# Optimization experiments

Measured on AMD Instinct MI355X. Metric: run time of the kernel, lower is better.

Reference implementation:

```python
import jax, jax.numpy as jnp
import numpy as np

E = 800_000      # number of edges
DIN = 128        # in_channels
DMID = 256       # mid_channels
DOUT = 128       # output_channels
V = 50_000       # number of vertices (segments)


def setup_inputs() -> dict:
    key = jax.random.key(0)
    k1, k2, k3, k4, k5 = jax.random.split(key, 5)
    x = jax.random.normal(k1, (E, DIN), dtype=jnp.float32)
    vertex_id = jax.random.randint(k2, (E,), 0, V)
    W1 = jax.random.normal(k3, (DIN, DMID), dtype=jnp.float32) * (1.0 / np.sqrt(DIN))
    b1 = jax.random.normal(k4, (DMID,), dtype=jnp.float32) * 0.01
    W2 = jax.random.normal(k5, (DIN + DMID, DOUT), dtype=jnp.float32) * (1.0 / np.sqrt(DIN + DMID))
    return {"x": x, "vertex_id": vertex_id, "W1": W1, "b1": b1, "W2": W2, "num_vertices": V}


def reference(x, vertex_id, W1, b1, W2, num_vertices):
    # first_process: Linear(DIN -> DMID)                        (E, DMID)
    z = x @ W1 + b1
    # aggregator: scatter_max over vertex segments              (V, DMID)
    z_max = jax.ops.segment_max(z, vertex_id, num_segments=num_vertices)
    # formatter: index_select gather back to edges              (E, DMID)
    z_vertex = jnp.take(z_max, vertex_id, axis=0)
    # merger: concat along feature dim                          (E, DIN+DMID)
    z_merged = jnp.concatenate([x, z_vertex], axis=-1)
    # second_process: Linear(DIN+DMID -> DOUT, bias=False)      (E, DOUT)
    return z_merged @ W2
```

## Files before the change

kernel.cpp:

```cpp
#include <hip/hip_runtime.h>

#define DIN   128
#define DMID  256
#define DOUT  128
#define VNUM  50000

typedef __attribute__((ext_vector_type(8))) __bf16 bf16x8;
typedef __attribute__((ext_vector_type(4))) float  f32x4;

static __device__ __forceinline__ unsigned flipf(float f) {
  unsigned u = __float_as_uint(f);
  return u ^ ((unsigned)((int)u >> 31) | 0x80000000u);
}
static __device__ __forceinline__ unsigned unflip_bits(unsigned m) {
  unsigned mask = ((int)m < 0) ? 0x80000000u : 0xFFFFFFFFu;
  return m ^ mask;
}
static __device__ __forceinline__ unsigned short flip16(unsigned short b) {
  return b ^ (unsigned short)(((short)b >> 15) | 0x8000);
}
static __device__ __forceinline__ unsigned flip32_from16(unsigned short m) {
  return ((unsigned)m << 16) | ((m & 0x8000u) ? 0u : 0xFFFFu);
}
static __device__ __forceinline__ unsigned short f2b_bits(unsigned b) {
  return (unsigned short)((b + 0x7FFFu + ((b >> 16) & 1u)) >> 16);
}
static __device__ __forceinline__ unsigned short f2b(float f) {
  return f2b_bits(__float_as_uint(f));
}

__global__ void k_hist(const int* __restrict__ vid, int* __restrict__ counts, int E) {
  int i = blockIdx.x * blockDim.x + threadIdx.x;
  if (i < E) atomicAdd(counts + vid[i], 1);
}

__global__ __launch_bounds__(1024) void k_scan(int* __restrict__ cursor, int V) {
  __shared__ int wsum[16];
  const int tid = threadIdx.x, lane = tid & 63, wv = tid >> 6;
  int carry = 0;
  for (int base = 0; base < V; base += 1024) {
    const int idx = base + tid;
    const int c = (idx < V) ? cursor[idx] : 0;
    int s = c;
#pragma unroll
    for (int d = 1; d < 64; d <<= 1) {
      int t = __shfl_up(s, d, 64);
      if (lane >= d) s += t;
    }
    if (lane == 63) wsum[wv] = s;
    __syncthreads();
    if (wv == 0 && lane < 16) {
      int ws = wsum[lane];
#pragma unroll
      for (int d = 1; d < 16; d <<= 1) {
        int t = __shfl_up(ws, d, 16);
        if (lane >= d) ws += t;
      }
      wsum[lane] = ws;
    }
    __syncthreads();
    const int woff = (wv == 0) ? 0 : wsum[wv - 1];
    if (idx < V) cursor[idx] = carry + woff + (s - c);
    carry += wsum[15];
    __syncthreads();
  }
}

__global__ void k_scatter(const int* __restrict__ vid, int* __restrict__ cursor,
                          int* __restrict__ sorted, int E) {
  int i = blockIdx.x * blockDim.x + threadIdx.x;
  if (i < E) {
    int v = vid[i];
    int p = atomicAdd(cursor + v, 1);
    sorted[p] = i;
  }
}

__global__ __launch_bounds__(256, 3) void k_gemm1_max(
    const float* __restrict__ x, const int* __restrict__ vid,
    const int* __restrict__ sorted, const float* __restrict__ W1,
    const float* __restrict__ b1, unsigned* __restrict__ zu, int ntiles) {
  __shared__ unsigned short lx[64 * 136];
  __shared__ unsigned short zt[64 * 266];
  __shared__ int lvid[64];
  __shared__ int leid[64];

  const int tid  = threadIdx.x;
  const int lane = tid & 63;
  const int w    = tid >> 6;
  const int l15  = lane & 15;
  const int l4   = lane >> 4;

  bf16x8 bfrag[4][4];
  float  bias[4];
#pragma unroll
  for (int ni = 0; ni < 4; ++ni) {
    const int col = w * 64 + ni * 16 + l15;
    bias[ni] = b1[col];
#pragma unroll
    for (int kk = 0; kk < 4; ++kk) {
      union { bf16x8 v; unsigned short u[8]; } tmp;
#pragma unroll
      for (int j = 0; j < 8; ++j)
        tmp.u[j] = f2b(W1[(kk * 32 + l4 * 8 + j) * DMID + col]);
      bfrag[kk][ni] = tmp.v;
    }
  }

  for (int t = blockIdx.x; t < ntiles; t += gridDim.x) {
    if (tid < 64) {
      const int e = sorted[t * 64 + tid];
      leid[tid] = e;
      lvid[tid] = vid[e];
    }
    __syncthreads();

    {
      const int row = tid >> 2, q = tid & 3;
      const float4* src =
          reinterpret_cast<const float4*>(x + (size_t)leid[row] * DIN + q * 32);
      unsigned short* dst = &lx[row * 136 + q * 32];
#pragma unroll
      for (int i = 0; i < 8; ++i) {
        float4 v = src[i];
        ushort4 o = { f2b(v.x), f2b(v.y), f2b(v.z), f2b(v.w) };
        *reinterpret_cast<ushort4*>(dst + i * 4) = o;
      }
    }
    __syncthreads();

    f32x4 acc[4][4];
#pragma unroll
    for (int mi = 0; mi < 4; ++mi)
#pragma unroll
      for (int ni = 0; ni < 4; ++ni)
        acc[mi][ni] = (f32x4){bias[ni], bias[ni], bias[ni], bias[ni]};
#pragma unroll
    for (int kk = 0; kk < 4; ++kk) {
      bf16x8 a[4];
#pragma unroll
      for (int mi = 0; mi < 4; ++mi)
        a[mi] = *reinterpret_cast<const bf16x8*>(
            &lx[(mi * 16 + l15) * 136 + kk * 32 + l4 * 8]);
#pragma unroll
      for (int mi = 0; mi < 4; ++mi)
#pragma unroll
        for (int ni = 0; ni < 4; ++ni)
          acc[mi][ni] = __builtin_amdgcn_mfma_f32_16x16x32_bf16(
              a[mi], bfrag[kk][ni], acc[mi][ni], 0, 0, 0);
    }

#pragma unroll
    for (int mi = 0; mi < 4; ++mi)
#pragma unroll
      for (int ni = 0; ni < 4; ++ni)
#pragma unroll
        for (int r = 0; r < 4; ++r) {
          const int row = mi * 16 + l4 * 4 + r;
          const int col = w * 64 + ni * 16 + l15;
          zt[row * 266 + col] = flip16(f2b(acc[mi][ni][r]));
        }
    __syncthreads();

    {
      const int col = tid;
      unsigned short cur = zt[col];
      int curv = lvid[0];
#pragma unroll 4
      for (int rr = 1; rr < 64; ++rr) {
        const unsigned short val = zt[rr * 266 + col];
        const int vv = lvid[rr];
        if (vv != curv) {
          atomicMax(zu + (size_t)curv * DMID + col, flip32_from16(cur));
          curv = vv;
          cur = val;
        } else {
          cur = (val > cur) ? val : cur;
        }
      }
      atomicMax(zu + (size_t)curv * DMID + col, flip32_from16(cur));
    }
    __syncthreads();
  }
}

__global__ __launch_bounds__(256) void k_ymm(
    const unsigned* __restrict__ zu, const float* __restrict__ W2,
    float* __restrict__ Y, int ntiles) {
  extern __shared__ unsigned short sm[];
  unsigned short* w2bt = sm;
  unsigned short* za   = sm + 128 * 264;

  const int tid  = threadIdx.x;
  const int lane = tid & 63;
  const int w    = tid >> 6;
  const int wr   = w >> 1, wc = w & 1;
  const int l15  = lane & 15, l4 = lane >> 4;

  {
    const int n = tid & 127, kh = tid >> 7;
    for (int k = kh * 128; k < kh * 128 + 128; ++k)
      w2bt[n * 264 + k] = f2b(W2[(size_t)(DIN + k) * DOUT + n]);
  }
  __syncthreads();

  for (int t = blockIdx.x; t < ntiles; t += gridDim.x) {
    {
      const int row = tid >> 2, q = tid & 3;
      const int v = t * 64 + row;
      unsigned short* dz = &za[row * 264 + q * 64];
      if (v < VNUM) {
        const uint4* sz = reinterpret_cast<const uint4*>(zu + (size_t)v * DMID + q * 64);
#pragma unroll
        for (int i = 0; i < 16; ++i) {
          uint4 m = sz[i];
          ushort4 o = { (unsigned short)(unflip_bits(m.x) >> 16),
                        (unsigned short)(unflip_bits(m.y) >> 16),
                        (unsigned short)(unflip_bits(m.z) >> 16),
                        (unsigned short)(unflip_bits(m.w) >> 16) };
          *reinterpret_cast<ushort4*>(dz + i * 4) = o;
        }
      } else {
        ushort4 zo = {0, 0, 0, 0};
#pragma unroll
        for (int i = 0; i < 16; ++i) *reinterpret_cast<ushort4*>(dz + i * 4) = zo;
      }
    }
    __syncthreads();

    f32x4 acc[2][4];
#pragma unroll
    for (int mi = 0; mi < 2; ++mi)
#pragma unroll
      for (int ni = 0; ni < 4; ++ni) acc[mi][ni] = (f32x4){0.f, 0.f, 0.f, 0.f};

#pragma unroll
    for (int kk = 0; kk < 8; ++kk) {
      bf16x8 a[2], b[4];
#pragma unroll
      for (int mi = 0; mi < 2; ++mi)
        a[mi] = *reinterpret_cast<const bf16x8*>(
            &za[(wr * 32 + mi * 16 + l15) * 264 + kk * 32 + l4 * 8]);
#pragma unroll
      for (int ni = 0; ni < 4; ++ni)
        b[ni] = *reinterpret_cast<const bf16x8*>(
            &w2bt[(wc * 64 + ni * 16 + l15) * 264 + kk * 32 + l4 * 8]);
#pragma unroll
      for (int mi = 0; mi < 2; ++mi)
#pragma unroll
        for (int ni = 0; ni < 4; ++ni)
          acc[mi][ni] = __builtin_amdgcn_mfma_f32_16x16x32_bf16(
              a[mi], b[ni], acc[mi][ni], 0, 0, 0);
    }

#pragma unroll
    for (int mi = 0; mi < 2; ++mi)
#pragma unroll
      for (int r = 0; r < 4; ++r) {
        const int v = t * 64 + wr * 32 + mi * 16 + l4 * 4 + r;
        if (v < VNUM) {
          float* o = Y + (size_t)v * DOUT + wc * 64 + l15;
#pragma unroll
          for (int ni = 0; ni < 4; ++ni) o[ni * 16] = acc[mi][ni][r];
        }
      }
    __syncthreads();
  }
}

__global__ __launch_bounds__(256, 3) void k_gemm2(
    const float* __restrict__ x, const int* __restrict__ vid,
    const float* __restrict__ W2, const float* __restrict__ Y,
    float* __restrict__ out, int ntiles) {
  __shared__ unsigned short w2at[128 * 136];
  __shared__ unsigned short lx[64 * 136];
  __shared__ int lvid[64];

  const int tid  = threadIdx.x;
  const int lane = tid & 63;
  const int w    = tid >> 6;
  const int wr   = w >> 1, wc = w & 1;
  const int l15  = lane & 15, l4 = lane >> 4;

  {
    const int n = tid & 127, kh = tid >> 7;
    for (int k = kh * 64; k < kh * 64 + 64; ++k)
      w2at[n * 136 + k] = f2b(W2[(size_t)k * DOUT + n]);
  }
  __syncthreads();

  for (int t = blockIdx.x; t < ntiles; t += gridDim.x) {
    {
      const int row = tid >> 2, q = tid & 3;
      const float4* sx =
          reinterpret_cast<const float4*>(x + (size_t)(t * 64 + row) * DIN + q * 32);
      unsigned short* dx = &lx[row * 136 + q * 32];
#pragma unroll
      for (int i = 0; i < 8; ++i) {
        float4 v = sx[i];
        ushort4 o = { f2b(v.x), f2b(v.y), f2b(v.z), f2b(v.w) };
        *reinterpret_cast<ushort4*>(dx + i * 4) = o;
      }
      if (tid < 64) lvid[tid] = vid[t * 64 + tid];
    }
    __syncthreads();

    f32x4 acc[2][4];
#pragma unroll
    for (int mi = 0; mi < 2; ++mi)
#pragma unroll
      for (int ni = 0; ni < 4; ++ni) acc[mi][ni] = (f32x4){0.f, 0.f, 0.f, 0.f};

#pragma unroll
    for (int kk = 0; kk < 4; ++kk) {
      bf16x8 a[2], b[4];
#pragma unroll
      for (int mi = 0; mi < 2; ++mi)
        a[mi] = *reinterpret_cast<const bf16x8*>(
            &lx[(wr * 32 + mi * 16 + l15) * 136 + kk * 32 + l4 * 8]);
#pragma unroll
      for (int ni = 0; ni < 4; ++ni)
        b[ni] = *reinterpret_cast<const bf16x8*>(
            &w2at[(wc * 64 + ni * 16 + l15) * 136 + kk * 32 + l4 * 8]);
#pragma unroll
      for (int mi = 0; mi < 2; ++mi)
#pragma unroll
        for (int ni = 0; ni < 4; ++ni)
          acc[mi][ni] = __builtin_amdgcn_mfma_f32_16x16x32_bf16(
              a[mi], b[ni], acc[mi][ni], 0, 0, 0);
    }

#pragma unroll
    for (int mi = 0; mi < 2; ++mi)
#pragma unroll
      for (int r = 0; r < 4; ++r) {
        const int row = wr * 32 + mi * 16 + l4 * 4 + r;
        const float* Yr = Y + (size_t)lvid[row] * DOUT + wc * 64 + l15;
        float* o = out + (size_t)(t * 64 + row) * DOUT + wc * 64 + l15;
#pragma unroll
        for (int ni = 0; ni < 4; ++ni) o[ni * 16] = acc[mi][ni][r] + Yr[ni * 16];
      }
    __syncthreads();
  }
}

extern "C" void kernel_launch(void* const* d_in, const int* in_sizes, int n_in,
                              void* d_out, int out_size, void* d_ws, size_t ws_size,
                              hipStream_t stream) {
  const float* x   = (const float*)d_in[0];
  const int*   vid = (const int*)d_in[1];
  const float* W1  = (const float*)d_in[2];
  const float* b1  = (const float*)d_in[3];
  const float* W2  = (const float*)d_in[4];
  float* out = (float*)d_out;

  const int E = in_sizes[1];
  const int ntiles = E / 64;
  const int ntY = (VNUM + 63) / 64;

  char* ws = (char*)d_ws;
  unsigned* zu   = (unsigned*)ws;
  int* cnt       = (int*)(ws + (size_t)VNUM * DMID * 4);
  int* sorted    = (int*)(ws + (size_t)VNUM * DMID * 4 + VNUM * 4);
  float* Y       = (float*)(ws + (size_t)VNUM * DMID * 4 + VNUM * 4 + (size_t)E * 4);

  hipMemsetAsync(zu, 0, (size_t)VNUM * DMID * 4 + VNUM * 4, stream);

  k_hist<<<(E + 255) / 256, 256, 0, stream>>>(vid, cnt, E);
  k_scan<<<1, 1024, 0, stream>>>(cnt, VNUM);
  k_scatter<<<(E + 255) / 256, 256, 0, stream>>>(vid, cnt, sorted, E);

  k_gemm1_max<<<768, 256, 0, stream>>>(x, vid, sorted, W1, b1, zu, ntiles);

  const int smY = (128 * 264 + 64 * 264) * sizeof(unsigned short);
  hipFuncSetAttribute((const void*)k_ymm,
                      hipFuncAttributeMaxDynamicSharedMemorySize, smY);
  k_ymm<<<256, 256, smY, stream>>>(zu, W2, Y, ntY);

  k_gemm2<<<768, 256, 0, stream>>>(x, vid, W2, Y, out, ntiles);
}
```

Baseline: 619.0 us.

## Prefetch next tile in registers and reduce segment max in registers

In both edge GEMM kernels, the next tile's x rows and vertex ids are now loaded into registers while the current tile's MFMAs run, so global-load latency overlaps compute. In gemm1 the segment max uses register fmax plus lane shuffles instead of staging through a shared z tile. Vertex runs that lie fully inside a tile are written with plain stores, and only runs at tile edges use atomicMax. The Y gather in gemm2 is hoisted ahead of the MFMAs, launch-bounds occupancy hints are dropped, and k_ymm gets enough blocks to cover all vertex tiles. The trade-off is higher register pressure, which may lower occupancy.

```diff
diff --git a/kernel.cpp b/kernel.cpp
--- a/kernel.cpp
+++ b/kernel.cpp
@@ -8,10 +8,6 @@
 typedef __attribute__((ext_vector_type(8))) __bf16 bf16x8;
 typedef __attribute__((ext_vector_type(4))) float  f32x4;
 
-static __device__ __forceinline__ unsigned flipf(float f) {
-  unsigned u = __float_as_uint(f);
-  return u ^ ((unsigned)((int)u >> 31) | 0x80000000u);
-}
 static __device__ __forceinline__ unsigned unflip_bits(unsigned m) {
   unsigned mask = ((int)m < 0) ? 0x80000000u : 0xFFFFFFFFu;
   return m ^ mask;
@@ -27,6 +23,9 @@
 }
 static __device__ __forceinline__ unsigned short f2b(float f) {
   return f2b_bits(__float_as_uint(f));
+}
+static __device__ __forceinline__ unsigned enc_max(float m) {
+  return flip32_from16(flip16(f2b(m)));
 }
 
 __global__ void k_hist(const int* __restrict__ vid, int* __restrict__ counts, int E) {
@@ -76,20 +75,21 @@
   }
 }
 
-__global__ __launch_bounds__(256, 3) void k_gemm1_max(
+__global__ __launch_bounds__(256) void k_gemm1_max(
     const float* __restrict__ x, const int* __restrict__ vid,
     const int* __restrict__ sorted, const float* __restrict__ W1,
     const float* __restrict__ b1, unsigned* __restrict__ zu, int ntiles) {
   __shared__ unsigned short lx[64 * 136];
-  __shared__ unsigned short zt[64 * 266];
   __shared__ int lvid[64];
-  __shared__ int leid[64];
 
   const int tid  = threadIdx.x;
   const int lane = tid & 63;
   const int w    = tid >> 6;
   const int l15  = lane & 15;
   const int l4   = lane >> 4;
+  const int row4 = tid >> 2;
+  const int q    = tid & 3;
+  const int G    = gridDim.x;
 
   bf16x8 bfrag[4][4];
   float  bias[4];
@@ -107,27 +107,36 @@
     }
   }
 
-  for (int t = blockIdx.x; t < ntiles; t += gridDim.x) {
-    if (tid < 64) {
-      const int e = sorted[t * 64 + tid];
-      leid[tid] = e;
-      lvid[tid] = vid[e];
-    }
-    __syncthreads();
-
-    {
-      const int row = tid >> 2, q = tid & 3;
-      const float4* src =
-          reinterpret_cast<const float4*>(x + (size_t)leid[row] * DIN + q * 32);
-      unsigned short* dst = &lx[row * 136 + q * 32];
-#pragma unroll
-      for (int i = 0; i < 8; ++i) {
-        float4 v = src[i];
-        ushort4 o = { f2b(v.x), f2b(v.y), f2b(v.z), f2b(v.w) };
-        *reinterpret_cast<ushort4*>(dst + i * 4) = o;
-      }
-    }
-    __syncthreads();
+  const int t0 = blockIdx.x;
+  if (t0 >= ntiles) return;
+
+  {
+    const int eid = sorted[t0 * 64 + row4];
+    const float4* src = reinterpret_cast<const float4*>(x + (size_t)eid * DIN + q * 32);
+    unsigned short* dst = &lx[row4 * 136 + q * 32];
+#pragma unroll
+    for (int i = 0; i < 8; ++i) {
+      float4 v = src[i];
+      ushort4 o = { f2b(v.x), f2b(v.y), f2b(v.z), f2b(v.w) };
+      *reinterpret_cast<ushort4*>(dst + i * 4) = o;
+    }
+    if (tid < 64) lvid[tid] = vid[sorted[t0 * 64 + tid]];
+  }
+  int tn0 = t0 + G; if (tn0 >= ntiles) tn0 = t0;
+  int eidN   = sorted[tn0 * 64 + row4];
+  int eidN64 = (tid < 64) ? sorted[tn0 * 64 + tid] : 0;
+  __syncthreads();
+
+  for (int t = t0; t < ntiles; t += G) {
+    int tn = t + G; if (tn >= ntiles) tn = t;
+
+    float4 xn[8];
+    {
+      const float4* src = reinterpret_cast<const float4*>(x + (size_t)eidN * DIN + q * 32);
+#pragma unroll
+      for (int i = 0; i < 8; ++i) xn[i] = src[i];
+    }
+    int vN = (tid < 64) ? vid[eidN64] : 0;
 
     f32x4 acc[4][4];
 #pragma unroll
@@ -150,36 +159,58 @@
               a[mi], bfrag[kk][ni], acc[mi][ni], 0, 0, 0);
     }
 
-#pragma unroll
-    for (int mi = 0; mi < 4; ++mi)
-#pragma unroll
-      for (int ni = 0; ni < 4; ++ni)
-#pragma unroll
-        for (int r = 0; r < 4; ++r) {
-          const int row = mi * 16 + l4 * 4 + r;
-          const int col = w * 64 + ni * 16 + l15;
-          zt[row * 266 + col] = flip16(f2b(acc[mi][ni][r]));
+    {
+      int rs = 0;
+      while (rs < 64) {
+        const int v = lvid[rs];
+        int re = rs + 1;
+        while (re < 64 && lvid[re] == v) ++re;
+
+        float mx[4];
+#pragma unroll
+        for (int ni = 0; ni < 4; ++ni) mx[ni] = -3.4e38f;
+#pragma unroll
+        for (int mi = 0; mi < 4; ++mi)
+#pragma unroll
+          for (int r = 0; r < 4; ++r) {
+            const int row = mi * 16 + l4 * 4 + r;
+            const bool in = (row >= rs) && (row < re);
+#pragma unroll
+            for (int ni = 0; ni < 4; ++ni)
+              mx[ni] = in ? fmaxf(mx[ni], acc[mi][ni][r]) : mx[ni];
+          }
+#pragma unroll
+        for (int ni = 0; ni < 4; ++ni) {
+          mx[ni] = fmaxf(mx[ni], __shfl_xor(mx[ni], 16));
+          mx[ni] = fmaxf(mx[ni], __shfl_xor(mx[ni], 32));
         }
-    __syncthreads();
-
-    {
-      const int col = tid;
-      unsigned short cur = zt[col];
-      int curv = lvid[0];
-#pragma unroll 4
-      for (int rr = 1; rr < 64; ++rr) {
-        const unsigned short val = zt[rr * 266 + col];
-        const int vv = lvid[rr];
-        if (vv != curv) {
-          atomicMax(zu + (size_t)curv * DMID + col, flip32_from16(cur));
-          curv = vv;
-          cur = val;
-        } else {
-          cur = (val > cur) ? val : cur;
+        const bool boundary = (rs == 0) || (re == 64);
+        if (l4 == 0) {
+          unsigned* base = zu + (size_t)v * DMID + w * 64 + l15;
+#pragma unroll
+          for (int ni = 0; ni < 4; ++ni) {
+            const unsigned e = enc_max(mx[ni]);
+            if (boundary) atomicMax(base + ni * 16, e);
+            else          base[ni * 16] = e;
+          }
         }
-      }
-      atomicMax(zu + (size_t)curv * DMID + col, flip32_from16(cur));
-    }
+        rs = re;
+      }
+    }
+    __syncthreads();
+
+    {
+      unsigned short* dst = &lx[row4 * 136 + q * 32];
+#pragma unroll
+      for (int i = 0; i < 8; ++i) {
+        ushort4 o = { f2b(xn[i].x), f2b(xn[i].y), f2b(xn[i].z), f2b(xn[i].w) };
+        *reinterpret_cast<ushort4*>(dst + i * 4) = o;
+      }
+      if (tid < 64) lvid[tid] = vN;
+    }
+    int t2 = tn + G; if (t2 >= ntiles) t2 = tn;
+    eidN   = sorted[t2 * 64 + row4];
+    eidN64 = (tid < 64) ? sorted[t2 * 64 + tid] : 0;
     __syncthreads();
   }
 }
@@ -268,7 +299,7 @@
   }
 }
 
-__global__ __launch_bounds__(256, 3) void k_gemm2(
+__global__ __launch_bounds__(256) void k_gemm2(
     const float* __restrict__ x, const int* __restrict__ vid,
     const float* __restrict__ W2, const float* __restrict__ Y,
     float* __restrict__ out, int ntiles) {
@@ -281,36 +312,65 @@
   const int w    = tid >> 6;
   const int wr   = w >> 1, wc = w & 1;
   const int l15  = lane & 15, l4 = lane >> 4;
+  const int row4 = tid >> 2, q = tid & 3;
+  const int G    = gridDim.x;
 
   {
     const int n = tid & 127, kh = tid >> 7;
     for (int k = kh * 64; k < kh * 64 + 64; ++k)
       w2at[n * 136 + k] = f2b(W2[(size_t)k * DOUT + n]);
   }
+
+  const int t0 = blockIdx.x;
+  if (t0 >= ntiles) return;
+
+  float4 xr[8];
+  {
+    const float4* src =
+        reinterpret_cast<const float4*>(x + (size_t)(t0 * 64 + row4) * DIN + q * 32);
+#pragma unroll
+    for (int i = 0; i < 8; ++i) xr[i] = src[i];
+  }
+  int vOwn = (tid < 64) ? vid[t0 * 64 + tid] : 0;
   __syncthreads();
 
-  for (int t = blockIdx.x; t < ntiles; t += gridDim.x) {
-    {
-      const int row = tid >> 2, q = tid & 3;
-      const float4* sx =
-          reinterpret_cast<const float4*>(x + (size_t)(t * 64 + row) * DIN + q * 32);
-      unsigned short* dx = &lx[row * 136 + q * 32];
+  for (int t = t0; t < ntiles; t += G) {
+    {
+      unsigned short* dst = &lx[row4 * 136 + q * 32];
 #pragma unroll
       for (int i = 0; i < 8; ++i) {
-        float4 v = sx[i];
-        ushort4 o = { f2b(v.x), f2b(v.y), f2b(v.z), f2b(v.w) };
-        *reinterpret_cast<ushort4*>(dx + i * 4) = o;
-      }
-      if (tid < 64) lvid[tid] = vid[t * 64 + tid];
-    }
-    __syncthreads();
+        ushort4 o = { f2b(xr[i].x), f2b(xr[i].y), f2b(xr[i].z), f2b(xr[i].w) };
+        *reinterpret_cast<ushort4*>(dst + i * 4) = o;
+      }
+      if (tid < 64) lvid[tid] = vOwn;
+    }
+    __syncthreads();
+
+    int tn = t + G; if (tn >= ntiles) tn = t;
+    {
+      const float4* src =
+          reinterpret_cast<const float4*>(x + (size_t)(tn * 64 + row4) * DIN + q * 32);
+#pragma unroll
+      for (int i = 0; i < 8; ++i) xr[i] = src[i];
+    }
+    vOwn = (tid < 64) ? vid[tn * 64 + tid] : 0;
+
+    float yv[2][4][4];
+#pragma unroll
+    for (int mi = 0; mi < 2; ++mi)
+#pragma unroll
+      for (int r = 0; r < 4; ++r) {
+        const int row = wr * 32 + mi * 16 + l4 * 4 + r;
+        const float* Yr = Y + (size_t)lvid[row] * DOUT + wc * 64 + l15;
+#pragma unroll
+        for (int ni = 0; ni < 4; ++ni) yv[mi][r][ni] = Yr[ni * 16];
+      }
 
     f32x4 acc[2][4];
 #pragma unroll
     for (int mi = 0; mi < 2; ++mi)
 #pragma unroll
       for (int ni = 0; ni < 4; ++ni) acc[mi][ni] = (f32x4){0.f, 0.f, 0.f, 0.f};
-
 #pragma unroll
     for (int kk = 0; kk < 4; ++kk) {
       bf16x8 a[2], b[4];
@@ -335,10 +395,9 @@
 #pragma unroll
       for (int r = 0; r < 4; ++r) {
         const int row = wr * 32 + mi * 16 + l4 * 4 + r;
-        const float* Yr = Y + (size_t)lvid[row] * DOUT + wc * 64 + l15;
         float* o = out + (size_t)(t * 64 + row) * DOUT + wc * 64 + l15;
 #pragma unroll
-        for (int ni = 0; ni < 4; ++ni) o[ni * 16] = acc[mi][ni][r] + Yr[ni * 16];
+        for (int ni = 0; ni < 4; ++ni) o[ni * 16] = acc[mi][ni][r] + yv[mi][r][ni];
       }
     __syncthreads();
   }
@@ -359,10 +418,10 @@
   const int ntY = (VNUM + 63) / 64;
 
   char* ws = (char*)d_ws;
-  unsigned* zu   = (unsigned*)ws;
-  int* cnt       = (int*)(ws + (size_t)VNUM * DMID * 4);
-  int* sorted    = (int*)(ws + (size_t)VNUM * DMID * 4 + VNUM * 4);
-  float* Y       = (float*)(ws + (size_t)VNUM * DMID * 4 + VNUM * 4 + (size_t)E * 4);
+  unsigned* zu = (unsigned*)ws;
+  int* cnt     = (int*)(ws + (size_t)VNUM * DMID * 4);
+  int* sorted  = (int*)(ws + (size_t)VNUM * DMID * 4 + VNUM * 4);
+  float* Y     = (float*)(ws + (size_t)VNUM * DMID * 4 + VNUM * 4 + (size_t)E * 4);
 
   hipMemsetAsync(zu, 0, (size_t)VNUM * DMID * 4 + VNUM * 4, stream);
 
@@ -375,7 +434,7 @@
   const int smY = (128 * 264 + 64 * 264) * sizeof(unsigned short);
   hipFuncSetAttribute((const void*)k_ymm,
                       hipFuncAttributeMaxDynamicSharedMemorySize, smY);
-  k_ymm<<<256, 256, smY, stream>>>(zu, W2, Y, ntY);
+  k_ymm<<<782, 256, smY, stream>>>(zu, W2, Y, ntY);
 
   k_gemm2<<<768, 256, 0, stream>>>(x, vid, W2, Y, out, ntiles);
 }
```

Result: slower. 939.0 us (+51.7%).

## Reduce segment max in registers via ballot runs and widen gemm1 blocks

Applied to the files above, without the earlier changes.

The first GEMM kernel now uses 512-thread blocks with 8 waves, each owning 32 output columns, and drops the LDS staging tile for the segment max. Segment boundaries are found with a wave ballot over the sorted vertex ids. Each run is reduced in registers with cross-lane shuffles, and interior runs are written with a plain store, while only runs touching the tile edges use atomicMax. The aim is to cut LDS traffic, a barrier and most of the atomics, at the cost of a serial loop over runs that is replicated in every wave. The grid sizes for gemm1 and k_ymm are also raised.

```diff
diff --git a/kernel.cpp b/kernel.cpp
--- a/kernel.cpp
+++ b/kernel.cpp
@@ -8,10 +8,6 @@
 typedef __attribute__((ext_vector_type(8))) __bf16 bf16x8;
 typedef __attribute__((ext_vector_type(4))) float  f32x4;
 
-static __device__ __forceinline__ unsigned flipf(float f) {
-  unsigned u = __float_as_uint(f);
-  return u ^ ((unsigned)((int)u >> 31) | 0x80000000u);
-}
 static __device__ __forceinline__ unsigned unflip_bits(unsigned m) {
   unsigned mask = ((int)m < 0) ? 0x80000000u : 0xFFFFFFFFu;
   return m ^ mask;
@@ -27,6 +23,9 @@
 }
 static __device__ __forceinline__ unsigned short f2b(float f) {
   return f2b_bits(__float_as_uint(f));
+}
+static __device__ __forceinline__ unsigned enc_max(float m) {
+  return flip32_from16(flip16(f2b(m)));
 }
 
 __global__ void k_hist(const int* __restrict__ vid, int* __restrict__ counts, int E) {
@@ -76,26 +75,26 @@
   }
 }
 
-__global__ __launch_bounds__(256, 3) void k_gemm1_max(
+__global__ __launch_bounds__(512, 4) void k_gemm1_max(
     const float* __restrict__ x, const int* __restrict__ vid,
     const int* __restrict__ sorted, const float* __restrict__ W1,
     const float* __restrict__ b1, unsigned* __restrict__ zu, int ntiles) {
   __shared__ unsigned short lx[64 * 136];
-  __shared__ unsigned short zt[64 * 266];
   __shared__ int lvid[64];
-  __shared__ int leid[64];
 
   const int tid  = threadIdx.x;
   const int lane = tid & 63;
   const int w    = tid >> 6;
   const int l15  = lane & 15;
   const int l4   = lane >> 4;
-
-  bf16x8 bfrag[4][4];
-  float  bias[4];
-#pragma unroll
-  for (int ni = 0; ni < 4; ++ni) {
-    const int col = w * 64 + ni * 16 + l15;
+  const int row8 = tid >> 3;
+  const int s8   = tid & 7;
+
+  bf16x8 bfrag[4][2];
+  float  bias[2];
+#pragma unroll
+  for (int ni = 0; ni < 2; ++ni) {
+    const int col = w * 32 + ni * 16 + l15;
     bias[ni] = b1[col];
 #pragma unroll
     for (int kk = 0; kk < 4; ++kk) {
@@ -108,20 +107,14 @@
   }
 
   for (int t = blockIdx.x; t < ntiles; t += gridDim.x) {
-    if (tid < 64) {
-      const int e = sorted[t * 64 + tid];
-      leid[tid] = e;
-      lvid[tid] = vid[e];
-    }
-    __syncthreads();
-
+    if (tid < 64) lvid[tid] = vid[sorted[t * 64 + tid]];
     {
-      const int row = tid >> 2, q = tid & 3;
+      const int eid = sorted[t * 64 + row8];
       const float4* src =
-          reinterpret_cast<const float4*>(x + (size_t)leid[row] * DIN + q * 32);
-      unsigned short* dst = &lx[row * 136 + q * 32];
-#pragma unroll
-      for (int i = 0; i < 8; ++i) {
+          reinterpret_cast<const float4*>(x + (size_t)eid * DIN + s8 * 16);
+      unsigned short* dst = &lx[row8 * 136 + s8 * 16];
+#pragma unroll
+      for (int i = 0; i < 4; ++i) {
         float4 v = src[i];
         ushort4 o = { f2b(v.x), f2b(v.y), f2b(v.z), f2b(v.w) };
         *reinterpret_cast<ushort4*>(dst + i * 4) = o;
@@ -129,11 +122,11 @@
     }
     __syncthreads();
 
-    f32x4 acc[4][4];
+    f32x4 acc[4][2];
 #pragma unroll
     for (int mi = 0; mi < 4; ++mi)
 #pragma unroll
-      for (int ni = 0; ni < 4; ++ni)
+      for (int ni = 0; ni < 2; ++ni)
         acc[mi][ni] = (f32x4){bias[ni], bias[ni], bias[ni], bias[ni]};
 #pragma unroll
     for (int kk = 0; kk < 4; ++kk) {
@@ -145,40 +138,45 @@
 #pragma unroll
       for (int mi = 0; mi < 4; ++mi)
 #pragma unroll
-        for (int ni = 0; ni < 4; ++ni)
+        for (int ni = 0; ni < 2; ++ni)
           acc[mi][ni] = __builtin_amdgcn_mfma_f32_16x16x32_bf16(
               a[mi], bfrag[kk][ni], acc[mi][ni], 0, 0, 0);
     }
 
-#pragma unroll
-    for (int mi = 0; mi < 4; ++mi)
-#pragma unroll
-      for (int ni = 0; ni < 4; ++ni)
-#pragma unroll
-        for (int r = 0; r < 4; ++r) {
-          const int row = mi * 16 + l4 * 4 + r;
-          const int col = w * 64 + ni * 16 + l15;
-          zt[row * 266 + col] = flip16(f2b(acc[mi][ni][r]));
+    {
+      const int myv = lvid[lane];
+      const int pv  = (lane == 0) ? ~myv : lvid[lane - 1];
+      unsigned long long m = __ballot(myv != pv);
+      while (m) {
+        const unsigned long long m2 = m & (m - 1);
+        const int rs = (int)__builtin_ctzll(m);
+        const int re = m2 ? (int)__builtin_ctzll(m2) : 64;
+
+        float mx0 = -3.4e38f, mx1 = -3.4e38f;
+#pragma unroll
+        for (int mi = 0; mi < 4; ++mi)
+#pragma unroll
+          for (int r = 0; r < 4; ++r) {
+            const int row = mi * 16 + l4 * 4 + r;
+            const bool in = (row >= rs) && (row < re);
+            mx0 = in ? fmaxf(mx0, acc[mi][0][r]) : mx0;
+            mx1 = in ? fmaxf(mx1, acc[mi][1][r]) : mx1;
+          }
+        mx0 = fmaxf(mx0, __shfl_xor(mx0, 16));
+        mx0 = fmaxf(mx0, __shfl_xor(mx0, 32));
+        mx1 = fmaxf(mx1, __shfl_xor(mx1, 16));
+        mx1 = fmaxf(mx1, __shfl_xor(mx1, 32));
+
+        const int v = lvid[rs];
+        const bool bd = (rs == 0) || (re == 64);
+        if (l4 == 0) {
+          unsigned* base = zu + (size_t)v * DMID + w * 32 + l15;
+          const unsigned e0 = enc_max(mx0), e1 = enc_max(mx1);
+          if (bd) { atomicMax(base, e0); atomicMax(base + 16, e1); }
+          else    { base[0] = e0;        base[16] = e1; }
         }
-    __syncthreads();
-
-    {
-      const int col = tid;
-      unsigned short cur = zt[col];
-      int curv = lvid[0];
-#pragma unroll 4
-      for (int rr = 1; rr < 64; ++rr) {
-        const unsigned short val = zt[rr * 266 + col];
-        const int vv = lvid[rr];
-        if (vv != curv) {
-          atomicMax(zu + (size_t)curv * DMID + col, flip32_from16(cur));
-          curv = vv;
-          cur = val;
-        } else {
-          cur = (val > cur) ? val : cur;
-        }
-      }
-      atomicMax(zu + (size_t)curv * DMID + col, flip32_from16(cur));
+        m = m2;
+      }
     }
     __syncthreads();
   }
@@ -359,10 +357,10 @@
   const int ntY = (VNUM + 63) / 64;
 
   char* ws = (char*)d_ws;
-  unsigned* zu   = (unsigned*)ws;
-  int* cnt       = (int*)(ws + (size_t)VNUM * DMID * 4);
-  int* sorted    = (int*)(ws + (size_t)VNUM * DMID * 4 + VNUM * 4);
-  float* Y       = (float*)(ws + (size_t)VNUM * DMID * 4 + VNUM * 4 + (size_t)E * 4);
+  unsigned* zu = (unsigned*)ws;
+  int* cnt     = (int*)(ws + (size_t)VNUM * DMID * 4);
+  int* sorted  = (int*)(ws + (size_t)VNUM * DMID * 4 + VNUM * 4);
+  float* Y     = (float*)(ws + (size_t)VNUM * DMID * 4 + VNUM * 4 + (size_t)E * 4);
 
   hipMemsetAsync(zu, 0, (size_t)VNUM * DMID * 4 + VNUM * 4, stream);
 
@@ -370,12 +368,12 @@
   k_scan<<<1, 1024, 0, stream>>>(cnt, VNUM);
   k_scatter<<<(E + 255) / 256, 256, 0, stream>>>(vid, cnt, sorted, E);
 
-  k_gemm1_max<<<768, 256, 0, stream>>>(x, vid, sorted, W1, b1, zu, ntiles);
+  k_gemm1_max<<<2048, 512, 0, stream>>>(x, vid, sorted, W1, b1, zu, ntiles);
 
   const int smY = (128 * 264 + 64 * 264) * sizeof(unsigned short);
   hipFuncSetAttribute((const void*)k_ymm,
                       hipFuncAttributeMaxDynamicSharedMemorySize, smY);
-  k_ymm<<<256, 256, smY, stream>>>(zu, W2, Y, ntY);
+  k_ymm<<<782, 256, smY, stream>>>(zu, W2, Y, ntY);
 
   k_gemm2<<<768, 256, 0, stream>>>(x, vid, W2, Y, out, ntiles);
 }
```

After: 694.6 us. +12.2%, slower.
